# Kernel tuning notes

Hardware: AMD Instinct MI355X
Metric: run time of the kernel (lower is better)

Reference implementation:

```python
import jax, jax.numpy as jnp
import numpy as np

HIDDEN = 1024
HEADS = 16
BATCH = 2
SEQ = 2048
# dropout_p = 0.1 but module evaluated in eval mode (training=False) -> identity


def setup_inputs() -> dict:
    key = jax.random.key(0)
    k1, k2, k3 = jax.random.split(key, 3)
    x = jax.random.normal(k1, (BATCH, SEQ, HIDDEN), dtype=jnp.float32)
    # unit-scaling Linear: weight ~ N(0,1) (reset_parameters uses nn.init.normal_)
    w_qkv = jax.random.normal(k2, (3 * HIDDEN, HIDDEN), dtype=jnp.float32)
    w_o = jax.random.normal(k3, (HIDDEN, HIDDEN), dtype=jnp.float32)
    return {"x": x, "w_qkv": w_qkv, "w_o": w_o}


def reference(x, w_qkv, w_o):
    b, s, hid = x.shape
    heads = HEADS
    d = hid // heads
    # unit-scaled linear (constraint='to_output_scale'): y = x @ W.T * fan_in**-0.5
    qkv = (x @ w_qkv.T) * (hid ** -0.5)            # [b, s, 3*hid]
    # einops 'b s (z h d) -> z b h s d'
    qkv = qkv.reshape(b, s, 3, heads, d)
    q = jnp.transpose(qkv[:, :, 0], (0, 2, 1, 3))   # [b, h, s, d]
    k = jnp.transpose(qkv[:, :, 1], (0, 2, 1, 3))
    v = jnp.transpose(qkv[:, :, 2], (0, 2, 1, 3))
    # unit-scaled matmul: scale = inner_dim**-0.5
    scores = jnp.einsum('bhqd,bhkd->bhqk', q, k) * (d ** -0.5)  # [b, h, s, s]
    # unit-scaled softmax: output_scale = n / sqrt(n - 1)
    attn = jax.nn.softmax(scores, axis=-1) * (s / np.sqrt(s - 1.0))
    # dropout inactive (eval mode)
    out = jnp.einsum('bhqk,bhkd->bhqd', attn, v) * (s ** -0.5)  # inner dim = s
    out = jnp.transpose(out, (0, 2, 1, 3)).reshape(b, s, hid)   # 'b h s d -> b s (h d)'
    return (out @ w_o.T) * (hid ** -0.5)
```

## Files before the change

### kernel.cpp

```cpp
#include <hip/hip_runtime.h>

typedef unsigned short u16;
typedef _Float16 f16x8 __attribute__((ext_vector_type(8)));
typedef _Float16 f16x4 __attribute__((ext_vector_type(4)));
typedef _Float16 f16x2 __attribute__((ext_vector_type(2)));
typedef float f32x4 __attribute__((ext_vector_type(4)));
typedef unsigned short u16x4 __attribute__((ext_vector_type(4)));

#define HID 1024
#define SEQ 2048
#define NH 16
#define DH 64

__device__ __forceinline__ u16 f2h(float f) {
  return __builtin_bit_cast(u16, (_Float16)f);
}
__device__ __forceinline__ f32x4 mfma_h(f16x8 a, f16x8 b, f32x4 c) {
  return __builtin_amdgcn_mfma_f32_16x16x32_f16(a, b, c, 0, 0, 0);
}
__device__ __forceinline__ f32x4 mfma_h16(f16x4 a, f16x4 b, f32x4 c) {
  return __builtin_amdgcn_mfma_f32_16x16x16f16(a, b, c, 0, 0, 0);
}
__device__ __forceinline__ float fexp2(float x) {
#if __has_builtin(__builtin_amdgcn_exp2f)
  return __builtin_amdgcn_exp2f(x);
#else
  return __expf(0.69314718f * x);
#endif
}
__device__ __forceinline__ f16x2 pkrtz(float a, float b) {
  return __builtin_bit_cast(f16x2, __builtin_amdgcn_cvt_pkrtz(a, b));
}
__device__ __forceinline__ void g2l16(const u16* g, u16* l) {
  __builtin_amdgcn_global_load_lds(
      (const __attribute__((address_space(1))) unsigned int*)g,
      (__attribute__((address_space(3))) unsigned int*)l, 16, 0, 0);
}

#define NX4 ((4096 * 1024) / 4)
#define NQ4 ((3072 * 1024) / 4)
#define NO4 ((1024 * 1024) / 4)
__global__ __launch_bounds__(256) void prep_kernel(
    const float* __restrict__ x, const float* __restrict__ wq,
    const float* __restrict__ wo,
    u16* __restrict__ x16, u16* __restrict__ wq16, u16* __restrict__ wo16) {
  int i = blockIdx.x * 256 + threadIdx.x;
  const float4 v = (i < NX4) ? ((const float4*)x)[i]
                 : (i < NX4 + NQ4) ? ((const float4*)wq)[i - NX4]
                 : ((const float4*)wo)[i - NX4 - NQ4];
  u16* dst = (i < NX4) ? &x16[(size_t)i * 4]
           : (i < NX4 + NQ4) ? &wq16[(size_t)(i - NX4) * 4]
           : &wo16[(size_t)(i - NX4 - NQ4) * 4];
  u16x4 o;
  o[0] = f2h(v.x); o[1] = f2h(v.y); o[2] = f2h(v.z); o[3] = f2h(v.w);
  *(u16x4*)dst = o;
}

__global__ __launch_bounds__(256, 3) void gemm_qkv(
    const u16* __restrict__ a16, const u16* __restrict__ b16,
    u16* __restrict__ qf, u16* __restrict__ kf, u16* __restrict__ vtf) {
  __shared__ __align__(16) u16 la[128 * 64], lb[128 * 64];
  const int t = threadIdx.x;
  const int lane = t & 63, w = t >> 6;
  const int wr = w >> 1, wc = w & 1;
  const int lr = lane & 15, lg = lane >> 4;
  const int br = blockIdx.x, bc = blockIdx.y;
  const f32x4 fzero = {0.f, 0.f, 0.f, 0.f};
  f32x4 acc[4][4];
#pragma unroll
  for (int i = 0; i < 4; ++i)
#pragma unroll
    for (int j = 0; j < 4; ++j) acc[i][j] = fzero;
  const int srow = t >> 3, scol = ((t & 7) ^ (srow & 7)) << 3;
  const u16* ga = a16 + (size_t)(br * 128 + srow) * HID + scol;
  const u16* gb = b16 + (size_t)(bc * 128 + srow) * HID + scol;
  const int lo16 = t * 8;
  for (int kk = 0; kk < HID; kk += 64) {
#pragma unroll
    for (int r = 0; r < 4; ++r)
      g2l16(ga + kk + (size_t)(r * 32) * HID, &la[lo16 + r * 2048]);
#pragma unroll
    for (int r = 0; r < 4; ++r)
      g2l16(gb + kk + (size_t)(r * 32) * HID, &lb[lo16 + r * 2048]);
    __syncthreads();
#pragma unroll
    for (int ks = 0; ks < 2; ++ks) {
      f16x8 ah[4], bh[4];
#pragma unroll
      for (int i = 0; i < 4; ++i) {
        int row = wr * 64 + i * 16 + lr;
        ah[i] = *(const f16x8*)&la[row * 64 + (((ks * 4 + lg) ^ (row & 7)) << 3)];
      }
#pragma unroll
      for (int j = 0; j < 4; ++j) {
        int row = wc * 64 + j * 16 + lr;
        bh[j] = *(const f16x8*)&lb[row * 64 + (((ks * 4 + lg) ^ (row & 7)) << 3)];
      }
#pragma unroll
      for (int i = 0; i < 4; ++i)
#pragma unroll
        for (int j = 0; j < 4; ++j) acc[i][j] = mfma_h(ah[i], bh[j], acc[i][j]);
    }
    __syncthreads();
  }
  const int m0 = br * 128 + wr * 64, n0 = bc * 128 + wc * 64;
#pragma unroll
  for (int i = 0; i < 4; ++i)
#pragma unroll
    for (int j = 0; j < 4; ++j)
#pragma unroll
      for (int r = 0; r < 4; ++r) {
        int row = m0 + i * 16 + lg * 4 + r;
        int col = n0 + j * 16 + lr;
        float val = acc[i][j][r] * 0.03125f;
        int b = row >> 11, s = row & 2047;
        int z = col >> 10, hh = (col >> 6) & 15, d = col & 63;
        int bhid = b * NH + hh;
        if (z == 0) {
          qf[((size_t)bhid * SEQ + s) * DH + d] = f2h(val * 0.18033688f);
        } else if (z == 1) {
          kf[((size_t)bhid * SEQ + s) * DH + d] = f2h(val);
        } else {
          int kv = s & 63;
          int ct = kv >> 4, lgv = (kv >> 2) & 3, rv = kv & 3;
          int kvp = ((ct >> 1) << 5) | (lgv << 3) | ((ct & 1) << 2) | rv;
          int s2 = (s & ~63) | kvp;
          vtf[((size_t)bhid * DH + d) * SEQ + s2] = f2h(val);
        }
      }
}

__global__ __launch_bounds__(256, 2) void gemm_proj(
    const u16* __restrict__ a16, const u16* __restrict__ b16,
    float* __restrict__ out) {
  __shared__ __align__(16) u16 la[128 * 64];
  __shared__ __align__(16) u16 lb[64 * 64];
  const int t = threadIdx.x;
  const int lane = t & 63, w = t >> 6;
  const int wr = w >> 1, wc = w & 1;
  const int lr = lane & 15, lg = lane >> 4;
  const int br = blockIdx.x, bc = blockIdx.y;
  const f32x4 fzero = {0.f, 0.f, 0.f, 0.f};
  f32x4 acc[4][2];
#pragma unroll
  for (int i = 0; i < 4; ++i)
#pragma unroll
    for (int j = 0; j < 2; ++j) acc[i][j] = fzero;
  const int srow = t >> 3, scol = ((t & 7) ^ (srow & 7)) << 3;
  const u16* ga = a16 + (size_t)(br * 128 + srow) * HID + scol;
  const u16* gb = b16 + (size_t)(bc * 64 + srow) * HID + scol;
  const int lo16 = t * 8;
  for (int kk = 0; kk < HID; kk += 64) {
#pragma unroll
    for (int r = 0; r < 4; ++r)
      g2l16(ga + kk + (size_t)(r * 32) * HID, &la[lo16 + r * 2048]);
#pragma unroll
    for (int r = 0; r < 2; ++r)
      g2l16(gb + kk + (size_t)(r * 32) * HID, &lb[lo16 + r * 2048]);
    __syncthreads();
#pragma unroll
    for (int ks = 0; ks < 2; ++ks) {
      f16x8 ah[4], bh[2];
#pragma unroll
      for (int i = 0; i < 4; ++i) {
        int row = wr * 64 + i * 16 + lr;
        ah[i] = *(const f16x8*)&la[row * 64 + (((ks * 4 + lg) ^ (row & 7)) << 3)];
      }
#pragma unroll
      for (int j = 0; j < 2; ++j) {
        int row = wc * 32 + j * 16 + lr;
        bh[j] = *(const f16x8*)&lb[row * 64 + (((ks * 4 + lg) ^ (row & 7)) << 3)];
      }
#pragma unroll
      for (int i = 0; i < 4; ++i)
#pragma unroll
        for (int j = 0; j < 2; ++j)
          acc[i][j] = mfma_h(ah[i], bh[j], acc[i][j]);
    }
    __syncthreads();
  }
  const int m0 = br * 128 + wr * 64, n0 = bc * 64 + wc * 32;
#pragma unroll
  for (int i = 0; i < 4; ++i)
#pragma unroll
    for (int j = 0; j < 2; ++j)
#pragma unroll
      for (int r = 0; r < 4; ++r) {
        int row = m0 + i * 16 + lg * 4 + r;
        int col = n0 + j * 16 + lr;
        out[(size_t)row * HID + col] = acc[i][j][r] * 0.03125f;
      }
}

__global__ __launch_bounds__(256, 2) void attn_kernel(
    const u16* __restrict__ qf, const u16* __restrict__ kf,
    const u16* __restrict__ vtf, u16* __restrict__ o16) {
  __shared__ __align__(16) u16 lk[2][64 * 64];
  __shared__ __align__(16) u16 lv[2][64 * 64];
  const int t = threadIdx.x;
  const int lane = t & 63, w = t >> 6;
  const int lr = lane & 15, lg = lane >> 4;
  const int bh = blockIdx.x, qt = blockIdx.y;
  const size_t base_qk = (size_t)bh * SEQ * DH;
  const size_t base_vt = (size_t)bh * DH * SEQ;

  f16x8 qfr[2][2];
#pragma unroll
  for (int rt = 0; rt < 2; ++rt)
#pragma unroll
    for (int ks = 0; ks < 2; ++ks)
      qfr[rt][ks] = *(const f16x8*)&qf[base_qk +
          (size_t)(qt * 128 + w * 32 + rt * 16 + lr) * DH + ks * 32 + lg * 8];

  f16x4 bI;
#pragma unroll
  for (int j = 0; j < 4; ++j) bI[j] = (_Float16)((lr == lg * 4 + j) ? 1.0f : 0.0f);
  f16x8 vones;
#pragma unroll
  for (int j = 0; j < 8; ++j) vones[j] = (_Float16)1.0f;

  const f32x4 fzero = {0.f, 0.f, 0.f, 0.f};
  f32x4 acc_o[2][4];
  f32x4 acc_l[2];
#pragma unroll
  for (int rt = 0; rt < 2; ++rt) {
    acc_l[rt] = fzero;
#pragma unroll
    for (int ct = 0; ct < 4; ++ct) acc_o[rt][ct] = fzero;
  }

  const int srow = t >> 3;
  const int scol = ((t & 7) ^ (srow & 7)) << 3;
  const int lo16 = t * 8;

  const u16* gk0 = kf + base_qk + (size_t)srow * DH + scol;
  const u16* gv0 = vtf + base_vt + (size_t)srow * SEQ + scol;

  auto STAGE_K = [&](int buf, int j) {
    const u16* gk = gk0 + (size_t)j * 64 * DH;
    g2l16(gk, &lk[buf][lo16]);
    g2l16(gk + 32 * DH, &lk[buf][lo16 + 2048]);
  };
  auto STAGE_V = [&](int buf, int j) {
    const u16* gv = gv0 + j * 64;
    g2l16(gv, &lv[buf][lo16]);
    g2l16(gv + (size_t)32 * SEQ, &lv[buf][lo16 + 2048]);
  };

  f32x4 saA[2][4], saB[2][4];

  auto QK_TILE = [&](f32x4 (&sa)[2][4], const u16* lkb) {
    __builtin_amdgcn_s_setprio(1);
#pragma unroll
    for (int ct = 0; ct < 4; ++ct) {
      int row = ct * 16 + lr;
      f16x8 k0 = *(const f16x8*)&lkb[row * 64 + ((lg ^ (row & 7)) << 3)];
      f16x8 k1 = *(const f16x8*)&lkb[row * 64 + (((4 + lg) ^ (row & 7)) << 3)];
      sa[0][ct] = mfma_h(qfr[0][0], k0, fzero);
      sa[1][ct] = mfma_h(qfr[1][0], k0, fzero);
      sa[0][ct] = mfma_h(qfr[0][1], k1, sa[0][ct]);
      sa[1][ct] = mfma_h(qfr[1][1], k1, sa[1][ct]);
    }
    __builtin_amdgcn_s_setprio(0);
  };

  auto SM_PV = [&](f32x4 (&sa)[2][4], const u16* lvb) {
    f16x8 pfr[2][2];
#pragma unroll
    for (int rt = 0; rt < 2; ++rt) {
      f32x4 tr[4];
#pragma unroll
      for (int ct = 0; ct < 4; ++ct) {
        float p0 = fexp2(sa[rt][ct][0]);
        float p1 = fexp2(sa[rt][ct][1]);
        float p2 = fexp2(sa[rt][ct][2]);
        float p3 = fexp2(sa[rt][ct][3]);
        union { f16x2 h2[2]; f16x4 h4; } ua;
        ua.h2[0] = pkrtz(p0, p1);
        ua.h2[1] = pkrtz(p2, p3);
        tr[ct] = mfma_h16(ua.h4, bI, fzero);
      }
#pragma unroll
      for (int ks = 0; ks < 2; ++ks) {
        union { f16x2 h2[4]; f16x8 h8; } up;
        up.h2[0] = pkrtz(tr[ks * 2][0], tr[ks * 2][1]);
        up.h2[1] = pkrtz(tr[ks * 2][2], tr[ks * 2][3]);
        up.h2[2] = pkrtz(tr[ks * 2 + 1][0], tr[ks * 2 + 1][1]);
        up.h2[3] = pkrtz(tr[ks * 2 + 1][2], tr[ks * 2 + 1][3]);
        pfr[rt][ks] = up.h8;
      }
    }
    __builtin_amdgcn_s_setprio(1);
#pragma unroll
    for (int ks = 0; ks < 2; ++ks)
#pragma unroll
      for (int ct = 0; ct < 4; ++ct) {
        int vrow = ct * 16 + lr;
        f16x8 vfr = *(const f16x8*)&lvb[vrow * 64 + (((ks * 4 + lg) ^ (vrow & 7)) << 3)];
#pragma unroll
        for (int rt = 0; rt < 2; ++rt) acc_o[rt][ct] = mfma_h(pfr[rt][ks], vfr, acc_o[rt][ct]);
      }
#pragma unroll
    for (int rt = 0; rt < 2; ++rt) {
      acc_l[rt] = mfma_h(pfr[rt][0], vones, acc_l[rt]);
      acc_l[rt] = mfma_h(pfr[rt][1], vones, acc_l[rt]);
    }
    __builtin_amdgcn_s_setprio(0);
  };

  STAGE_K(0, 0);
  STAGE_V(0, 0);
  STAGE_K(1, 1);
  __syncthreads();
  QK_TILE(saA, lk[0]);

  for (int n = 0; n < 30; n += 2) {
    __syncthreads();
    STAGE_V(1, n + 1);
    STAGE_K(0, n + 2);
    QK_TILE(saB, lk[1]);
    SM_PV(saA, lv[0]);

    __syncthreads();
    STAGE_V(0, n + 2);
    STAGE_K(1, n + 3);
    QK_TILE(saA, lk[0]);
    SM_PV(saB, lv[1]);
  }
  __syncthreads();
  STAGE_V(1, 31);
  QK_TILE(saB, lk[1]);
  SM_PV(saA, lv[0]);
  __syncthreads();
  SM_PV(saB, lv[1]);

  const int b = bh >> 4, hh = bh & 15;
  const float fact = 1.00024426f;
#pragma unroll
  for (int rt = 0; rt < 2; ++rt)
#pragma unroll
    for (int r = 0; r < 4; ++r) {
      float inv = fact / acc_l[rt][r];
      int s = qt * 128 + w * 32 + rt * 16 + lg * 4 + r;
#pragma unroll
      for (int ct = 0; ct < 4; ++ct) {
        int d = ct * 16 + lr;
        float val = acc_o[rt][ct][r] * inv;
        o16[((size_t)(b * SEQ + s)) * HID + hh * DH + d] = f2h(val);
      }
    }
}

extern "C" void kernel_launch(void* const* d_in, const int* in_sizes, int n_in,
                              void* d_out, int out_size, void* d_ws, size_t ws_size,
                              hipStream_t stream) {
  const float* x = (const float*)d_in[0];
  const float* w_qkv = (const float*)d_in[1];
  const float* w_o = (const float*)d_in[2];
  u16* ws = (u16*)d_ws;
  const size_t XS = (size_t)4096 * 1024;
  const size_t WQ = (size_t)3072 * 1024;
  const size_t WO = (size_t)1024 * 1024;
  u16* x16  = ws;           u16* wq16 = x16 + XS;
  u16* wo16 = wq16 + WQ;
  u16* q_f  = wo16 + WO;    u16* k_f  = q_f + XS;
  u16* vt_f = k_f + XS;     u16* o16  = vt_f + XS;

  prep_kernel<<<(NX4 + NQ4 + NO4) / 256, 256, 0, stream>>>(
      x, w_qkv, w_o, x16, wq16, wo16);
  gemm_qkv<<<dim3(32, 24), 256, 0, stream>>>(x16, wq16, q_f, k_f, vt_f);
  attn_kernel<<<dim3(32, 16), 256, 0, stream>>>(q_f, k_f, vt_f, o16);
  gemm_proj<<<dim3(32, 16), 256, 0, stream>>>(o16, wo16, (float*)d_out);
}
```

Before: 177.1 us.

## Split attention over two KV halves and merge partials in projection GEMM

The attention kernel now splits the key/value sequence into two halves across a third grid dimension, doubling the block count, and raises the occupancy hint to 4 blocks per SU. Each half writes unnormalised fp16 partial outputs and row sums, and the output projection GEMM sums the two partials, normalises them and converts to fp16 while staging its A operand into LDS. This relies on no running-max rescaling, since scores are pre-scaled, so the partials combine by simple addition. The goal is better GPU occupancy for attention, at the cost of extra partial-output traffic, synchronous loads in place of async copies in gemm_proj, and reuse of the x16 and wq16 workspace buffers.

```diff
diff --git a/kernel.cpp b/kernel.cpp
--- a/kernel.cpp
+++ b/kernel.cpp
@@ -131,10 +131,12 @@
 }
 
 __global__ __launch_bounds__(256, 2) void gemm_proj(
-    const u16* __restrict__ a16, const u16* __restrict__ b16,
+    const u16* __restrict__ po0, const u16* __restrict__ po1,
+    const float* __restrict__ pl, const u16* __restrict__ b16,
     float* __restrict__ out) {
   __shared__ __align__(16) u16 la[128 * 64];
   __shared__ __align__(16) u16 lb[64 * 64];
+  __shared__ float linv[16 * 128];
   const int t = threadIdx.x;
   const int lane = t & 63, w = t >> 6;
   const int wr = w >> 1, wc = w & 1;
@@ -146,17 +148,39 @@
   for (int i = 0; i < 4; ++i)
 #pragma unroll
     for (int j = 0; j < 2; ++j) acc[i][j] = fzero;
+#pragma unroll
+  for (int jj = 0; jj < 8; ++jj) {
+    int idx = t + jj * 256;
+    int h = idx >> 7, i = idx & 127;
+    int ar = br * 128 + i;
+    int b = ar >> 11, s = ar & 2047;
+    int bhs = (b * NH + h) * SEQ + s;
+    linv[idx] = 1.00024426f / (pl[bhs] + pl[NH * 2 * SEQ + bhs]);
+  }
+  __syncthreads();
   const int srow = t >> 3, scol = ((t & 7) ^ (srow & 7)) << 3;
-  const u16* ga = a16 + (size_t)(br * 128 + srow) * HID + scol;
+  const u16* gp0 = po0 + (size_t)(br * 128 + srow) * HID + scol;
+  const u16* gp1 = po1 + (size_t)(br * 128 + srow) * HID + scol;
   const u16* gb = b16 + (size_t)(bc * 64 + srow) * HID + scol;
   const int lo16 = t * 8;
   for (int kk = 0; kk < HID; kk += 64) {
 #pragma unroll
-    for (int r = 0; r < 4; ++r)
-      g2l16(ga + kk + (size_t)(r * 32) * HID, &la[lo16 + r * 2048]);
-#pragma unroll
     for (int r = 0; r < 2; ++r)
       g2l16(gb + kk + (size_t)(r * 32) * HID, &lb[lo16 + r * 2048]);
+#pragma unroll
+    for (int r = 0; r < 4; ++r) {
+      f16x8 a0 = *(const f16x8*)(gp0 + kk + (size_t)(r * 32) * HID);
+      f16x8 a1 = *(const f16x8*)(gp1 + kk + (size_t)(r * 32) * HID);
+      float invr = linv[((kk >> 6) << 7) + srow + r * 32];
+      union { f16x2 h2[4]; f16x8 h8; } uo;
+#pragma unroll
+      for (int p = 0; p < 4; ++p) {
+        float s0 = ((float)a0[2 * p] + (float)a1[2 * p]) * invr;
+        float s1 = ((float)a0[2 * p + 1] + (float)a1[2 * p + 1]) * invr;
+        uo.h2[p] = pkrtz(s0, s1);
+      }
+      *(f16x8*)&la[lo16 + r * 2048] = uo.h8;
+    }
     __syncthreads();
 #pragma unroll
     for (int ks = 0; ks < 2; ++ks) {
@@ -192,15 +216,16 @@
       }
 }
 
-__global__ __launch_bounds__(256, 2) void attn_kernel(
+__global__ __launch_bounds__(256, 4) void attn_kernel(
     const u16* __restrict__ qf, const u16* __restrict__ kf,
-    const u16* __restrict__ vtf, u16* __restrict__ o16) {
+    const u16* __restrict__ vtf, u16* __restrict__ po0,
+    u16* __restrict__ po1, float* __restrict__ pl) {
   __shared__ __align__(16) u16 lk[2][64 * 64];
   __shared__ __align__(16) u16 lv[2][64 * 64];
   const int t = threadIdx.x;
   const int lane = t & 63, w = t >> 6;
   const int lr = lane & 15, lg = lane >> 4;
-  const int bh = blockIdx.x, qt = blockIdx.y;
+  const int bh = blockIdx.x, qt = blockIdx.y, sp = blockIdx.z;
   const size_t base_qk = (size_t)bh * SEQ * DH;
   const size_t base_vt = (size_t)bh * DH * SEQ;
 
@@ -233,8 +258,8 @@
   const int scol = ((t & 7) ^ (srow & 7)) << 3;
   const int lo16 = t * 8;
 
-  const u16* gk0 = kf + base_qk + (size_t)srow * DH + scol;
-  const u16* gv0 = vtf + base_vt + (size_t)srow * SEQ + scol;
+  const u16* gk0 = kf + base_qk + (size_t)(sp * 1024 + srow) * DH + scol;
+  const u16* gv0 = vtf + base_vt + (size_t)srow * SEQ + sp * 1024 + scol;
 
   auto STAGE_K = [&](int buf, int j) {
     const u16* gk = gk0 + (size_t)j * 64 * DH;
@@ -314,7 +339,7 @@
   __syncthreads();
   QK_TILE(saA, lk[0]);
 
-  for (int n = 0; n < 30; n += 2) {
+  for (int n = 0; n < 14; n += 2) {
     __syncthreads();
     STAGE_V(1, n + 1);
     STAGE_K(0, n + 2);
@@ -328,25 +353,26 @@
     SM_PV(saB, lv[1]);
   }
   __syncthreads();
-  STAGE_V(1, 31);
+  STAGE_V(1, 15);
   QK_TILE(saB, lk[1]);
   SM_PV(saA, lv[0]);
   __syncthreads();
   SM_PV(saB, lv[1]);
 
   const int b = bh >> 4, hh = bh & 15;
-  const float fact = 1.00024426f;
+  u16* pob = sp ? po1 : po0;
+  float* plb = pl + sp * (NH * 2 * SEQ);
 #pragma unroll
   for (int rt = 0; rt < 2; ++rt)
 #pragma unroll
     for (int r = 0; r < 4; ++r) {
-      float inv = fact / acc_l[rt][r];
       int s = qt * 128 + w * 32 + rt * 16 + lg * 4 + r;
+      int row = b * SEQ + s;
+      if (lr == 0) plb[bh * SEQ + s] = acc_l[rt][r];
 #pragma unroll
       for (int ct = 0; ct < 4; ++ct) {
         int d = ct * 16 + lr;
-        float val = acc_o[rt][ct][r] * inv;
-        o16[((size_t)(b * SEQ + s)) * HID + hh * DH + d] = f2h(val);
+        pob[(size_t)row * HID + hh * DH + d] = f2h(acc_o[rt][ct][r]);
       }
     }
 }
@@ -364,11 +390,13 @@
   u16* x16  = ws;           u16* wq16 = x16 + XS;
   u16* wo16 = wq16 + WQ;
   u16* q_f  = wo16 + WO;    u16* k_f  = q_f + XS;
-  u16* vt_f = k_f + XS;     u16* o16  = vt_f + XS;
+  u16* vt_f = k_f + XS;     u16* po0  = vt_f + XS;
+  u16* po1  = x16;
+  float* pl = (float*)wq16;
 
   prep_kernel<<<(NX4 + NQ4 + NO4) / 256, 256, 0, stream>>>(
       x, w_qkv, w_o, x16, wq16, wo16);
   gemm_qkv<<<dim3(32, 24), 256, 0, stream>>>(x16, wq16, q_f, k_f, vt_f);
-  attn_kernel<<<dim3(32, 16), 256, 0, stream>>>(q_f, k_f, vt_f, o16);
-  gemm_proj<<<dim3(32, 16), 256, 0, stream>>>(o16, wo16, (float*)d_out);
-}
+  attn_kernel<<<dim3(32, 16, 2), 256, 0, stream>>>(q_f, k_f, vt_f, po0, po1, pl);
+  gemm_proj<<<dim3(32, 16), 256, 0, stream>>>(po0, po1, pl, wo16, (float*)d_out);
+}
```

Result: slower. 244.6 us (+38.2%).
